# Kernel tuning notes

Measured on AMD Instinct MI355X. Metric: run time of the kernel, lower is better.

The kernel has to match this reference:

```python
import jax, jax.numpy as jnp
import numpy as np

DIM = 1024
HEADS = 16
DIM_HEAD = 64
EPS = 1e-5


def setup_inputs() -> dict:
    key = jax.random.key(0)
    ks = jax.random.split(key, 8)
    s = 1.0 / np.sqrt(DIM)
    return {
        "x": jax.random.normal(ks[0], (4, 2048, DIM), dtype=jnp.float32),
        "ln_w": jnp.ones((DIM,), jnp.float32),
        "ln_b": jnp.zeros((DIM,), jnp.float32),
        "wq": jax.random.normal(ks[1], (DIM, DIM), jnp.float32) * s,
        "bq": jax.random.normal(ks[2], (DIM,), jnp.float32) * s,
        "wk": jax.random.normal(ks[3], (DIM, DIM), jnp.float32) * s,
        "bk": jax.random.normal(ks[4], (DIM,), jnp.float32) * s,
        "wv": jax.random.normal(ks[5], (DIM, DIM), jnp.float32) * s,
        "bv": jax.random.normal(ks[6], (DIM,), jnp.float32) * s,
    }


def _split_heads(t):
    b, n, _ = t.shape
    return t.reshape(b, n, HEADS, DIM_HEAD).transpose(0, 2, 1, 3)  # b h n d


def reference(x, ln_w, ln_b, wq, bq, wk, bk, wv, bv):
    # LayerNorm over last dim
    mu = jnp.mean(x, axis=-1, keepdims=True)
    var = jnp.mean(jnp.square(x - mu), axis=-1, keepdims=True)
    h = (x - mu) * jax.lax.rsqrt(var + EPS) * ln_w + ln_b

    q = _split_heads(h @ wq + bq)
    k = _split_heads(h @ wk + bk)
    v = _split_heads(h @ wv + bv)

    scale = 1.0 / jnp.sqrt(jnp.float32(DIM_HEAD))
    scores = jnp.einsum('bhnd,bhmd->bhnm', q, k) * scale
    att = jax.nn.softmax(scores, axis=-1)
    out = jnp.einsum('bhnm,bhmd->bhnd', att, v)
    b, _, n, _ = out.shape
    return out.transpose(0, 2, 1, 3).reshape(b, n, HEADS * DIM_HEAD)
```

## Files before the change

### kernel.cpp

```cpp
#include <hip/hip_runtime.h>
#include <hip/hip_bf16.h>
#include <stdint.h>

#define DIM    1024
#define HEADS  16
#define DHEAD  64
#define SEQ    2048
#define BATCH  4

typedef unsigned short u16;
typedef __attribute__((ext_vector_type(4))) float f32x4;
typedef __attribute__((ext_vector_type(8))) short bf16x8;

#define QSCALE 0.18033688011112042f

__device__ inline u16 f2bf(float f) {
  __hip_bfloat16 h = __float2bfloat16(f);
  return *reinterpret_cast<u16*>(&h);
}

__device__ inline void async_load16(const void* g, void* l) {
  __builtin_amdgcn_global_load_lds((const __attribute__((address_space(1))) void*)g,
                                   (__attribute__((address_space(3))) void*)l, 16, 0, 0);
}

__global__ __launch_bounds__(256) void ln_kernel(const float* __restrict__ x,
                                                 const float* __restrict__ w,
                                                 const float* __restrict__ b,
                                                 u16* __restrict__ h) {
  int row = blockIdx.x;
  int t = threadIdx.x;
  const float4* xr = (const float4*)(x + (size_t)row * DIM);
  float4 v = xr[t];
  float s  = v.x + v.y + v.z + v.w;
  float s2 = v.x*v.x + v.y*v.y + v.z*v.z + v.w*v.w;
  for (int m = 1; m < 64; m <<= 1) { s += __shfl_xor(s, m); s2 += __shfl_xor(s2, m); }
  __shared__ float ss[4], ss2[4];
  int wid = t >> 6;
  if ((t & 63) == 0) { ss[wid] = s; ss2[wid] = s2; }
  __syncthreads();
  s  = ss[0] + ss[1] + ss[2] + ss[3];
  s2 = ss2[0] + ss2[1] + ss2[2] + ss2[3];
  float mu  = s * (1.0f / DIM);
  float var = s2 * (1.0f / DIM) - mu * mu;
  float rs  = rsqrtf(var + 1e-5f);
  float4 wv4 = ((const float4*)w)[t];
  float4 bv4 = ((const float4*)b)[t];
  ushort4 o;
  o.x = f2bf((v.x - mu) * rs * wv4.x + bv4.x);
  o.y = f2bf((v.y - mu) * rs * wv4.y + bv4.y);
  o.z = f2bf((v.z - mu) * rs * wv4.z + bv4.z);
  o.w = f2bf((v.w - mu) * rs * wv4.w + bv4.w);
  ((ushort4*)(h + (size_t)row * DIM))[t] = o;
}

__global__ __launch_bounds__(256) void wt_kernel(const float* __restrict__ wq,
                                                 const float* __restrict__ wk,
                                                 const float* __restrict__ wv,
                                                 u16* __restrict__ wt) {
  int mat = blockIdx.z;
  const float* w = (mat == 0) ? wq : ((mat == 1) ? wk : wv);
  __shared__ float tile[32][33];
  int j0 = blockIdx.x * 32, d0 = blockIdx.y * 32;
  int tc = threadIdx.x & 31, tr = threadIdx.x >> 5;
  for (int i = 0; i < 32; i += 8)
    tile[tr + i][tc] = w[(size_t)(d0 + tr + i) * DIM + j0 + tc];
  __syncthreads();
  u16* dst = wt + (size_t)mat * DIM * DIM;
  for (int i = 0; i < 32; i += 8)
    dst[(size_t)(j0 + tr + i) * DIM + d0 + tc] = f2bf(tile[tc][tr + i]);
}

__global__ __launch_bounds__(256) void gemm_qkv(const u16* __restrict__ A,
                                                const u16* __restrict__ Bt,
                                                const float* __restrict__ bq,
                                                const float* __restrict__ bk,
                                                const float* __restrict__ bv,
                                                u16* __restrict__ qo,
                                                u16* __restrict__ ko,
                                                u16* __restrict__ vo) {
  __shared__ u16 lA[128 * 32];
  __shared__ u16 lB[128 * 32];
  int t = threadIdx.x;
  int bm = blockIdx.x, bn = blockIdx.y;
  const u16* Ab = A + (size_t)bm * 128 * DIM;
  const u16* Bb = Bt + (size_t)bn * 128 * DIM;
  int lane = t & 63, w = t >> 6;
  int wm = (w >> 1) * 64, wn = (w & 1) * 64;
  int fr = lane & 15;
  int fk = (lane >> 4) * 8;
  f32x4 acc[4][4];
  for (int i = 0; i < 4; ++i) for (int j = 0; j < 4; ++j) acc[i][j] = (f32x4)(0.0f);

  for (int k0 = 0; k0 < DIM; k0 += 32) {
    __syncthreads();
    for (int r = 0; r < 2; ++r) {
      int flat = (t + r * 256) * 8;
      int m = flat >> 5, kk = flat & 31;
      async_load16(Ab + (size_t)m * DIM + k0 + kk, lA + flat);
      async_load16(Bb + (size_t)m * DIM + k0 + kk, lB + flat);
    }
    __syncthreads();
    bf16x8 af[4], bfm[4];
    for (int i = 0; i < 4; ++i) af[i]  = *(const bf16x8*)(lA + (wm + i * 16 + fr) * 32 + fk);
    for (int i = 0; i < 4; ++i) bfm[i] = *(const bf16x8*)(lB + (wn + i * 16 + fr) * 32 + fk);
    for (int i = 0; i < 4; ++i)
      for (int j = 0; j < 4; ++j)
        acc[i][j] = __builtin_amdgcn_mfma_f32_16x16x32_bf16(af[i], bfm[j], acc[i][j], 0, 0, 0);
  }

  int quad = lane >> 4;
  for (int j = 0; j < 4; ++j) {
    int gn = bn * 128 + wn + j * 16 + fr;
    int mat = gn >> 10, c = gn & 1023;
    const float* bias = (mat == 0) ? bq : ((mat == 1) ? bk : bv);
    float bb = bias[c];
    int head = c >> 6, d = c & 63;
    for (int i = 0; i < 4; ++i) {
      for (int r = 0; r < 4; ++r) {
        int gm = bm * 128 + wm + i * 16 + quad * 4 + r;
        int b = gm >> 11, n = gm & 2047;
        float val = acc[i][j][r] + bb;
        size_t bhbase = (size_t)(b * HEADS + head) * SEQ * DHEAD;
        if (mat == 0) {
          qo[bhbase + (size_t)n * DHEAD + d] = f2bf(val * QSCALE);
        } else if (mat == 1) {
          ko[bhbase + (size_t)(n >> 7) * 8192 + (size_t)(n & 127) * 64
             + (((d >> 3) ^ (n & 7)) << 3) + (d & 7)] = f2bf(val);
        } else {
          vo[bhbase + (size_t)(n >> 7) * 8192 + (size_t)d * 128
             + ((((n & 127) >> 3) ^ (d & 15)) << 3) + (n & 7)] = f2bf(val);
        }
      }
    }
  }
}

__global__ __launch_bounds__(256, 2) void flash_attn(const u16* __restrict__ Q,
                                                     const u16* __restrict__ Ksw,
                                                     const u16* __restrict__ Vsw,
                                                     float* __restrict__ out) {
  __shared__ __align__(16) u16 smem[8192 + 8192 + 128 * 136];
  u16* lK  = smem;
  u16* lVt = smem + 8192;
  u16* lP  = smem + 16384;
  u16* lQ  = lP;

  int t = threadIdx.x;
  int lane = t & 63, w = t >> 6;
  int wrow = w * 32;
  int fr = lane & 15, quad = lane >> 4, fk = quad * 8;
  int qtile = blockIdx.x, bh = blockIdx.y;
  int b = bh >> 4, head = bh & 15;

  const u16* Qb  = Q   + ((size_t)bh * SEQ + qtile * 128) * DHEAD;
  const u16* Kbh = Ksw + (size_t)bh * SEQ * DHEAD;
  const u16* Vbh = Vsw + (size_t)bh * SEQ * DHEAD;

  for (int p = 0; p < 4; ++p) {
    int flat = (t + p * 256) * 8;
    async_load16(Qb + flat, lQ + flat);
  }
  __syncthreads();
  bf16x8 aq[2][2];
  for (int mi = 0; mi < 2; ++mi)
    for (int ks = 0; ks < 2; ++ks)
      aq[mi][ks] = *(const bf16x8*)(lQ + (wrow + mi * 16 + fr) * 64 + ks * 32 + fk);

  f32x4 O[4][2];
  for (int nd = 0; nd < 4; ++nd) for (int mi = 0; mi < 2; ++mi) O[nd][mi] = (f32x4)(0.0f);
  float mold[2] = {-1e30f, -1e30f};
  float lsum[2] = {0.0f, 0.0f};

  for (int it = 0; it < 16; ++it) {
    __syncthreads();
    const u16* Kb = Kbh + (size_t)it * 8192;
    const u16* Vb = Vbh + (size_t)it * 8192;
    for (int p = 0; p < 4; ++p) {
      int flat = (t + p * 256) * 8;
      async_load16(Kb + flat, lK + flat);
      async_load16(Vb + flat, lVt + flat);
    }
    __syncthreads();

    f32x4 T[8][2];
    for (int ni = 0; ni < 8; ++ni) for (int mi = 0; mi < 2; ++mi) T[ni][mi] = (f32x4)(0.0f);
#pragma unroll
    for (int ni = 0; ni < 8; ++ni) {
      int kv = ni * 16 + fr;
      int sw = kv & 7;
#pragma unroll
      for (int ks = 0; ks < 2; ++ks) {
        bf16x8 kb = *(const bf16x8*)(lK + kv * 64 + (((ks * 4 + quad) ^ sw) << 3));
        T[ni][0] = __builtin_amdgcn_mfma_f32_16x16x32_bf16(kb, aq[0][ks], T[ni][0], 0, 0, 0);
        T[ni][1] = __builtin_amdgcn_mfma_f32_16x16x32_bf16(kb, aq[1][ks], T[ni][1], 0, 0, 0);
      }
    }

#pragma unroll
    for (int mi = 0; mi < 2; ++mi) {
      float mx = T[0][mi][0];
#pragma unroll
      for (int ni = 0; ni < 8; ++ni)
#pragma unroll
        for (int r = 0; r < 4; ++r) mx = fmaxf(mx, T[ni][mi][r]);
      mx = fmaxf(mx, __shfl_xor(mx, 16));
      mx = fmaxf(mx, __shfl_xor(mx, 32));
      float mn = fmaxf(mold[mi], mx);
      float al = __builtin_amdgcn_exp2f(mold[mi] - mn);
      mold[mi] = mn;
      int qrow = wrow + mi * 16 + fr;
      float s = 0.0f;
#pragma unroll
      for (int ni = 0; ni < 8; ++ni) {
        float p0 = __builtin_amdgcn_exp2f(T[ni][mi][0] - mn);
        float p1 = __builtin_amdgcn_exp2f(T[ni][mi][1] - mn);
        float p2 = __builtin_amdgcn_exp2f(T[ni][mi][2] - mn);
        float p3 = __builtin_amdgcn_exp2f(T[ni][mi][3] - mn);
        s += (p0 + p1) + (p2 + p3);
        uint2 pk;
        pk.x = (uint32_t)f2bf(p0) | ((uint32_t)f2bf(p1) << 16);
        pk.y = (uint32_t)f2bf(p2) | ((uint32_t)f2bf(p3) << 16);
        *(uint2*)(lP + (size_t)qrow * 136 + ni * 16 + quad * 4) = pk;
      }
      s += __shfl_xor(s, 16);
      s += __shfl_xor(s, 32);
      lsum[mi] = lsum[mi] * al + s;
#pragma unroll
      for (int nd = 0; nd < 4; ++nd)
#pragma unroll
        for (int r = 0; r < 4; ++r) O[nd][mi][r] *= al;
    }

#pragma unroll
    for (int ks = 0; ks < 4; ++ks) {
      bf16x8 pa[2];
#pragma unroll
      for (int mi = 0; mi < 2; ++mi)
        pa[mi] = *(const bf16x8*)(lP + (size_t)(wrow + mi * 16 + fr) * 136 + ks * 32 + fk);
#pragma unroll
      for (int nd = 0; nd < 4; ++nd) {
        int d = nd * 16 + fr;
        bf16x8 vb = *(const bf16x8*)(lVt + d * 128 + (((ks * 4 + quad) ^ (d & 15)) << 3));
        O[nd][0] = __builtin_amdgcn_mfma_f32_16x16x32_bf16(vb, pa[0], O[nd][0], 0, 0, 0);
        O[nd][1] = __builtin_amdgcn_mfma_f32_16x16x32_bf16(vb, pa[1], O[nd][1], 0, 0, 0);
      }
    }
  }

  float* ob = out + ((size_t)b * SEQ + qtile * 128) * DIM + head * DHEAD;
#pragma unroll
  for (int mi = 0; mi < 2; ++mi) {
    float inv = 1.0f / lsum[mi];
    int q = wrow + mi * 16 + fr;
#pragma unroll
    for (int nd = 0; nd < 4; ++nd) {
      float4 vv;
      vv.x = O[nd][mi][0] * inv;
      vv.y = O[nd][mi][1] * inv;
      vv.z = O[nd][mi][2] * inv;
      vv.w = O[nd][mi][3] * inv;
      *(float4*)(ob + (size_t)q * DIM + nd * 16 + quad * 4) = vv;
    }
  }
}

extern "C" void kernel_launch(void* const* d_in, const int* in_sizes, int n_in,
                              void* d_out, int out_size, void* d_ws, size_t ws_size,
                              hipStream_t stream) {
  const float* x   = (const float*)d_in[0];
  const float* lnw = (const float*)d_in[1];
  const float* lnb = (const float*)d_in[2];
  const float* wq  = (const float*)d_in[3];
  const float* bq  = (const float*)d_in[4];
  const float* wk  = (const float*)d_in[5];
  const float* bk  = (const float*)d_in[6];
  const float* wv  = (const float*)d_in[7];
  const float* bv  = (const float*)d_in[8];
  float* out = (float*)d_out;

  char* ws = (char*)d_ws;
  u16* h  = (u16*)(ws);
  u16* wt = (u16*)(ws + 16777216);
  u16* q  = (u16*)(ws + 23068672);
  u16* k  = (u16*)(ws + 39845888);
  u16* v  = (u16*)(ws + 56623104);

  ln_kernel<<<8192, 256, 0, stream>>>(x, lnw, lnb, h);
  wt_kernel<<<dim3(32, 32, 3), 256, 0, stream>>>(wq, wk, wv, wt);
  gemm_qkv<<<dim3(64, 24), 256, 0, stream>>>(h, wt, bq, bk, bv, q, k, v);
  flash_attn<<<dim3(16, 64), 256, 0, stream>>>(q, k, v, out);
}
```

Baseline: 300.1 us.

## Keep softmax probabilities in registers via permuted V layout; widen GEMM K-tile with swizzle

The attention kernel now packs the bf16 probabilities straight into MFMA operand registers instead of writing them to shared memory and reading them back. To make that valid, the QKV GEMM epilogue stores V in a permuted key order that matches the register layout. Dropping the P buffer shrinks shared memory, so occupancy is raised to 3 blocks per SM. The GEMM also moves from a K-tile of 32 to 64, with XOR-swizzled LDS to avoid bank conflicts.

```diff
diff --git a/kernel.cpp b/kernel.cpp
--- a/kernel.cpp
+++ b/kernel.cpp
@@ -17,6 +17,10 @@
 __device__ inline u16 f2bf(float f) {
   __hip_bfloat16 h = __float2bfloat16(f);
   return *reinterpret_cast<u16*>(&h);
+}
+
+__device__ inline uint32_t pack_bf16(float lo, float hi) {
+  return (uint32_t)f2bf(lo) | ((uint32_t)f2bf(hi) << 16);
 }
 
 __device__ inline void async_load16(const void* g, void* l) {
@@ -79,8 +83,8 @@
                                                 u16* __restrict__ qo,
                                                 u16* __restrict__ ko,
                                                 u16* __restrict__ vo) {
-  __shared__ u16 lA[128 * 32];
-  __shared__ u16 lB[128 * 32];
+  __shared__ u16 lA[128 * 64];
+  __shared__ u16 lB[128 * 64];
   int t = threadIdx.x;
   int bm = blockIdx.x, bn = blockIdx.y;
   const u16* Ab = A + (size_t)bm * 128 * DIM;
@@ -88,28 +92,42 @@
   int lane = t & 63, w = t >> 6;
   int wm = (w >> 1) * 64, wn = (w & 1) * 64;
   int fr = lane & 15;
-  int fk = (lane >> 4) * 8;
+  int quad = lane >> 4;
   f32x4 acc[4][4];
   for (int i = 0; i < 4; ++i) for (int j = 0; j < 4; ++j) acc[i][j] = (f32x4)(0.0f);
 
-  for (int k0 = 0; k0 < DIM; k0 += 32) {
+  for (int k0 = 0; k0 < DIM; k0 += 64) {
     __syncthreads();
-    for (int r = 0; r < 2; ++r) {
+#pragma unroll
+    for (int r = 0; r < 4; ++r) {
       int flat = (t + r * 256) * 8;
-      int m = flat >> 5, kk = flat & 31;
-      async_load16(Ab + (size_t)m * DIM + k0 + kk, lA + flat);
-      async_load16(Bb + (size_t)m * DIM + k0 + kk, lB + flat);
+      int m = flat >> 6, c = (flat >> 3) & 7;
+      int gk = k0 + ((c ^ (m & 7)) << 3);
+      async_load16(Ab + (size_t)m * DIM + gk, lA + flat);
+      async_load16(Bb + (size_t)m * DIM + gk, lB + flat);
     }
     __syncthreads();
-    bf16x8 af[4], bfm[4];
-    for (int i = 0; i < 4; ++i) af[i]  = *(const bf16x8*)(lA + (wm + i * 16 + fr) * 32 + fk);
-    for (int i = 0; i < 4; ++i) bfm[i] = *(const bf16x8*)(lB + (wn + i * 16 + fr) * 32 + fk);
-    for (int i = 0; i < 4; ++i)
-      for (int j = 0; j < 4; ++j)
-        acc[i][j] = __builtin_amdgcn_mfma_f32_16x16x32_bf16(af[i], bfm[j], acc[i][j], 0, 0, 0);
-  }
-
-  int quad = lane >> 4;
+#pragma unroll
+    for (int ks = 0; ks < 2; ++ks) {
+      bf16x8 af[4], bfm[4];
+#pragma unroll
+      for (int i = 0; i < 4; ++i) {
+        int m = wm + i * 16 + fr;
+        af[i] = *(const bf16x8*)(lA + m * 64 + (((ks * 4 + quad) ^ (fr & 7)) << 3));
+      }
+#pragma unroll
+      for (int i = 0; i < 4; ++i) {
+        int m = wn + i * 16 + fr;
+        bfm[i] = *(const bf16x8*)(lB + m * 64 + (((ks * 4 + quad) ^ (fr & 7)) << 3));
+      }
+#pragma unroll
+      for (int i = 0; i < 4; ++i)
+#pragma unroll
+        for (int j = 0; j < 4; ++j)
+          acc[i][j] = __builtin_amdgcn_mfma_f32_16x16x32_bf16(af[i], bfm[j], acc[i][j], 0, 0, 0);
+    }
+  }
+
   for (int j = 0; j < 4; ++j) {
     int gn = bn * 128 + wn + j * 16 + fr;
     int mat = gn >> 10, c = gn & 1023;
@@ -128,23 +146,25 @@
           ko[bhbase + (size_t)(n >> 7) * 8192 + (size_t)(n & 127) * 64
              + (((d >> 3) ^ (n & 7)) << 3) + (d & 7)] = f2bf(val);
         } else {
+          int n127 = n & 127;
+          int kv5 = n127 & 31;
+          int s = (n127 & 96) | ((kv5 & 12) << 1) | ((kv5 & 16) >> 2) | (kv5 & 3);
           vo[bhbase + (size_t)(n >> 7) * 8192 + (size_t)d * 128
-             + ((((n & 127) >> 3) ^ (d & 15)) << 3) + (n & 7)] = f2bf(val);
+             + (((s >> 3) ^ (d & 15)) << 3) + (s & 7)] = f2bf(val);
         }
       }
     }
   }
 }
 
-__global__ __launch_bounds__(256, 2) void flash_attn(const u16* __restrict__ Q,
+__global__ __launch_bounds__(256, 3) void flash_attn(const u16* __restrict__ Q,
                                                      const u16* __restrict__ Ksw,
                                                      const u16* __restrict__ Vsw,
                                                      float* __restrict__ out) {
-  __shared__ __align__(16) u16 smem[8192 + 8192 + 128 * 136];
+  __shared__ __align__(16) u16 smem[8192 + 8192];
   u16* lK  = smem;
   u16* lVt = smem + 8192;
-  u16* lP  = smem + 16384;
-  u16* lQ  = lP;
+  u16* lQ  = smem;
 
   int t = threadIdx.x;
   int lane = t & 63, w = t >> 6;
@@ -176,6 +196,7 @@
     __syncthreads();
     const u16* Kb = Kbh + (size_t)it * 8192;
     const u16* Vb = Vbh + (size_t)it * 8192;
+#pragma unroll
     for (int p = 0; p < 4; ++p) {
       int flat = (t + p * 256) * 8;
       async_load16(Kb + flat, lK + flat);
@@ -184,6 +205,7 @@
     __syncthreads();
 
     f32x4 T[8][2];
+#pragma unroll
     for (int ni = 0; ni < 8; ++ni) for (int mi = 0; mi < 2; ++mi) T[ni][mi] = (f32x4)(0.0f);
 #pragma unroll
     for (int ni = 0; ni < 8; ++ni) {
@@ -197,6 +219,7 @@
       }
     }
 
+    uint32_t pkA[8][2], pkB[8][2];
 #pragma unroll
     for (int mi = 0; mi < 2; ++mi) {
       float mx = T[0][mi][0];
@@ -209,7 +232,6 @@
       float mn = fmaxf(mold[mi], mx);
       float al = __builtin_amdgcn_exp2f(mold[mi] - mn);
       mold[mi] = mn;
-      int qrow = wrow + mi * 16 + fr;
       float s = 0.0f;
 #pragma unroll
       for (int ni = 0; ni < 8; ++ni) {
@@ -218,10 +240,8 @@
         float p2 = __builtin_amdgcn_exp2f(T[ni][mi][2] - mn);
         float p3 = __builtin_amdgcn_exp2f(T[ni][mi][3] - mn);
         s += (p0 + p1) + (p2 + p3);
-        uint2 pk;
-        pk.x = (uint32_t)f2bf(p0) | ((uint32_t)f2bf(p1) << 16);
-        pk.y = (uint32_t)f2bf(p2) | ((uint32_t)f2bf(p3) << 16);
-        *(uint2*)(lP + (size_t)qrow * 136 + ni * 16 + quad * 4) = pk;
+        pkA[ni][mi] = pack_bf16(p0, p1);
+        pkB[ni][mi] = pack_bf16(p2, p3);
       }
       s += __shfl_xor(s, 16);
       s += __shfl_xor(s, 32);
@@ -236,8 +256,14 @@
     for (int ks = 0; ks < 4; ++ks) {
       bf16x8 pa[2];
 #pragma unroll
-      for (int mi = 0; mi < 2; ++mi)
-        pa[mi] = *(const bf16x8*)(lP + (size_t)(wrow + mi * 16 + fr) * 136 + ks * 32 + fk);
+      for (int mi = 0; mi < 2; ++mi) {
+        union { uint32_t u[4]; bf16x8 v; } cvt;
+        cvt.u[0] = pkA[2 * ks][mi];
+        cvt.u[1] = pkB[2 * ks][mi];
+        cvt.u[2] = pkA[2 * ks + 1][mi];
+        cvt.u[3] = pkB[2 * ks + 1][mi];
+        pa[mi] = cvt.v;
+      }
 #pragma unroll
       for (int nd = 0; nd < 4; ++nd) {
         int d = nd * 16 + fr;
```

After: 272.7 us. 1.1x faster.
